# Optimization experiments

Hardware: AMD Instinct MI355X
Metric: run time of the kernel (lower is better)

The kernel has to match this reference:

```python
import jax, jax.numpy as jnp
import numpy as np

D_MODEL = 1024

def setup_inputs() -> dict:
    key = jax.random.key(0)
    ks = jax.random.split(key, 7)
    B, S, D = 4, 2048, D_MODEL
    scale = 1.0 / np.sqrt(D)
    x = jax.random.normal(ks[0], (B, S, D), dtype=jnp.float32)
    Wq = jax.random.normal(ks[1], (D, D), dtype=jnp.float32) * scale
    bq = jnp.zeros((D,), dtype=jnp.float32)
    Wk = jax.random.normal(ks[2], (D, D), dtype=jnp.float32) * scale
    bk = jnp.zeros((D,), dtype=jnp.float32)
    Wv = jax.random.normal(ks[3], (D, D), dtype=jnp.float32) * scale
    bv = jnp.zeros((D,), dtype=jnp.float32)
    return {"x": x, "Wq": Wq, "bq": bq, "Wk": Wk, "bk": bk, "Wv": Wv, "bv": bv}

def reference(x, Wq, bq, Wk, bk, Wv, bv):
    # Single-head attention; scale = 1/sqrt(d_model) as in the torch module (self.d_k = d_model).
    d_k = x.shape[-1]
    q = jnp.einsum('bsd,de->bse', x, Wq) + bq
    k = jnp.einsum('bsd,de->bse', x, Wk) + bk
    v = jnp.einsum('bsd,de->bse', x, Wv) + bv
    scores = jnp.einsum('bqd,bkd->bqk', q, k) / jnp.sqrt(jnp.asarray(d_k, x.dtype))
    attn = jax.nn.softmax(scores, axis=-1)
    return jnp.einsum('bqk,bkd->bqd', attn, v)
```

## Files before the change

kernel.cpp:

```cpp
#include <hip/hip_runtime.h>
#include <hip/hip_bf16.h>

#define DM 1024
#define SEQ 2048
#define NBATCH 4

using f32x4 = __attribute__((ext_vector_type(4))) float;
using s16x8 = __attribute__((ext_vector_type(8))) short;
using u16x4 = __attribute__((ext_vector_type(4))) unsigned short;
using u16x8 = __attribute__((ext_vector_type(8))) unsigned short;

__device__ __forceinline__ unsigned short f2bf(float f) {
  union { float f; unsigned u; } v; v.f = f;
  return (unsigned short)((v.u + 0x7fffu + ((v.u >> 16) & 1u)) >> 16);
}

__device__ __forceinline__ void gll16(const unsigned short* g, unsigned short* l) {
  __builtin_amdgcn_global_load_lds((const __attribute__((address_space(1))) void*)g,
                                   (__attribute__((address_space(3))) void*)l,
                                   16, 0, 0);
}

__global__ void prep_k(const float* __restrict__ X,
                       const float* __restrict__ Wq, const float* __restrict__ Wk,
                       const float* __restrict__ Wv,
                       unsigned short* __restrict__ XB, unsigned short* __restrict__ WT) {
  __shared__ float t[32][33];
  const int b = blockIdx.x;
  if (b < 4096) {
    const int i = b * 256 + threadIdx.x;
    const f32x4* p = (const f32x4*)X;
    f32x4 a = p[2 * i], c = p[2 * i + 1];
    u16x8 o;
#pragma unroll
    for (int q = 0; q < 4; q++) { o[q] = f2bf(a[q]); o[4 + q] = f2bf(c[q]); }
    *(u16x8*)(XB + (size_t)i * 8) = o;
  } else {
    const int r2 = b - 4096;
    const int seg = r2 >> 10;
    const int rem = r2 & 1023;
    const int k0 = (rem >> 5) * 32, n0 = (rem & 31) * 32;
    const float* W = (seg == 0) ? Wq : (seg == 1) ? Wk : Wv;
    unsigned short* out = WT + (size_t)seg * DM * DM;
    const int tr = threadIdx.x >> 5, tc = threadIdx.x & 31;
#pragma unroll
    for (int p = 0; p < 4; p++) {
      int r = tr + p * 8;
      t[r][tc] = W[(size_t)(k0 + r) * DM + n0 + tc];
    }
    __syncthreads();
#pragma unroll
    for (int p = 0; p < 4; p++) {
      int r = tr + p * 8;
      out[(size_t)(n0 + r) * DM + k0 + tc] = f2bf(t[tc][r]);
    }
  }
}

__global__ void combine_k(const float* __restrict__ ms, const float* __restrict__ ss,
                          float* __restrict__ T) {
  const int idx = blockIdx.x * 256 + threadIdx.x;
  const float* m = ms + (size_t)idx * 16;
  const float* s = ss + (size_t)idx * 32;
  float mv[16];
#pragma unroll
  for (int t = 0; t < 16; t++) mv[t] = m[t];
  float M = mv[0];
#pragma unroll
  for (int t = 1; t < 16; t++) M = fmaxf(M, mv[t]);
  float L = 0.f;
#pragma unroll
  for (int t = 0; t < 16; t++) L += (s[2 * t] + s[2 * t + 1]) * __expf(mv[t] - M);
  T[idx] = 1.0f;
#pragma unroll
  for (int t = 1; t < 16; t++) T[t * 8192 + idx] = __expf(mv[t - 1] - mv[t]);
  T[16 * 8192 + idx] = __expf(mv[15] - M) / L;
}

__global__ __launch_bounds__(512, 2) void qkv8_k(
    const unsigned short* __restrict__ A,
    const unsigned short* __restrict__ B,
    unsigned short* __restrict__ Qo, unsigned short* __restrict__ Ko,
    unsigned short* __restrict__ Vt,
    const float* __restrict__ bq, const float* __restrict__ bk,
    const float* __restrict__ bv) {
  constexpr int NKS = 32;
  __shared__ unsigned short lds8[65536];
  unsigned short* lA = lds8;
  unsigned short* lB = lds8 + 32768;

  const int tid = threadIdx.x;
  const int w = tid >> 6, l = tid & 63;
  const int ll = l & 15, qd = l >> 4;
  const int wm = w & 1, wn = w >> 1;

  const int bid = blockIdx.x;
  const int xcd = bid & 7, slot = bid >> 3;
  const int mt = xcd * 4 + slot / 12;
  const int nt = slot % 12;
  const int tileM = mt * 256, tileN = nt * 256;

  const int seg = l >> 3, ch = l & 7;
  const int rowo = seg * 2 + (ch >> 2);
  const int kc = (ch & 3) ^ (seg & 3);
  const unsigned short* gA0 = A + (size_t)(tileM + w * 16 + rowo) * DM + kc * 8;
  const unsigned short* gA1 = gA0 + (size_t)128 * DM;
  const unsigned short* gB0 = B + (size_t)(tileN + w * 16 + rowo) * DM + kc * 8;
  const unsigned short* gB1 = gB0 + (size_t)128 * DM;
  const int dA0 = w * 512, dA1 = (w + 8) * 512;

#define STAGE_A(n_) do { unsigned short* d_ = lA + ((n_) & 3) * 8192;          \
    gll16(gA0 + (size_t)(n_) * 32, d_ + dA0);                                  \
    gll16(gA1 + (size_t)(n_) * 32, d_ + dA1); } while (0)
#define STAGE_B(n_) do { unsigned short* d_ = lB + ((n_) & 3) * 8192;          \
    gll16(gB0 + (size_t)(n_) * 32, d_ + dA0);                                  \
    gll16(gB1 + (size_t)(n_) * 32, d_ + dA1); } while (0)

  const int Ra = wm * 128 + ll;
  const int aoff = (Ra >> 1) * 64 + ((Ra & 1) * 4 + (qd ^ ((Ra >> 1) & 3))) * 8;
  const int Rb = wn * 64 + ll;
  const int boff = (Rb >> 1) * 64 + ((Rb & 1) * 4 + (qd ^ ((Rb >> 1) & 3))) * 8;

  f32x4 acc[8][4];
#pragma unroll
  for (int i = 0; i < 8; i++)
#pragma unroll
    for (int j = 0; j < 4; j++) acc[i][j] = (f32x4){0.f, 0.f, 0.f, 0.f};

  STAGE_A(0); STAGE_B(0); STAGE_A(1); STAGE_B(1); STAGE_A(2); STAGE_B(2); STAGE_B(3);
  __builtin_amdgcn_sched_barrier(0);
  __builtin_amdgcn_s_waitcnt(0x0F7A);
  __builtin_amdgcn_sched_barrier(0);
  __builtin_amdgcn_s_barrier();
  __builtin_amdgcn_sched_barrier(0);

  for (int n = 0; n < NKS; ++n) {
    const unsigned short* sA = lA + (n & 3) * 8192;
    const unsigned short* sB = lB + (n & 3) * 8192;
    s16x8 af[4], bf[4];

#pragma unroll
    for (int i = 0; i < 4; i++) af[i] = *(const s16x8*)&sA[aoff + i * 512];
#pragma unroll
    for (int j = 0; j < 4; j++) bf[j] = *(const s16x8*)&sB[boff + j * 512];
    if (n + 3 < NKS) STAGE_A(n + 3);
    __builtin_amdgcn_sched_barrier(0);
    __builtin_amdgcn_s_barrier();
    __builtin_amdgcn_s_waitcnt(0xC07F);
    __builtin_amdgcn_sched_barrier(0);
    __builtin_amdgcn_s_setprio(1);
#pragma unroll
    for (int i = 0; i < 4; i++)
#pragma unroll
      for (int j = 0; j < 4; j++)
        acc[i][j] = __builtin_amdgcn_mfma_f32_16x16x32_bf16(af[i], bf[j], acc[i][j], 0, 0, 0);
    __builtin_amdgcn_s_setprio(0);
    __builtin_amdgcn_sched_barrier(0);
    __builtin_amdgcn_s_barrier();
    __builtin_amdgcn_sched_barrier(0);

#pragma unroll
    for (int i = 0; i < 4; i++) af[i] = *(const s16x8*)&sA[aoff + (i + 4) * 512];
    if (n + 4 < NKS) STAGE_B(n + 4);
    __builtin_amdgcn_sched_barrier(0);
    __builtin_amdgcn_s_barrier();
    __builtin_amdgcn_s_waitcnt(0xC07F);
    __builtin_amdgcn_sched_barrier(0);
    __builtin_amdgcn_s_setprio(1);
#pragma unroll
    for (int i = 0; i < 4; i++)
#pragma unroll
      for (int j = 0; j < 4; j++)
        acc[i + 4][j] = __builtin_amdgcn_mfma_f32_16x16x32_bf16(af[i], bf[j], acc[i + 4][j], 0, 0, 0);
    __builtin_amdgcn_s_setprio(0);
    if (n < NKS - 4)       __builtin_amdgcn_s_waitcnt(0x0F7A);
    else if (n == NKS - 4) __builtin_amdgcn_s_waitcnt(0x0F78);
    else if (n == NKS - 3) __builtin_amdgcn_s_waitcnt(0x0F74);
    else if (n == NKS - 2) __builtin_amdgcn_s_waitcnt(0x0F70);
    __builtin_amdgcn_sched_barrier(0);
    __builtin_amdgcn_s_barrier();
    __builtin_amdgcn_sched_barrier(0);
  }
#undef STAGE_A
#undef STAGE_B

#pragma unroll
  for (int i = 0; i < 8; i++) {
    const int gm0 = tileM + wm * 128 + i * 16 + qd * 4;
#pragma unroll
    for (int j = 0; j < 4; j++) {
      const int gn = tileN + wn * 64 + j * 16 + ll;
      const int seg2 = gn >> 10;
      const int colin = gn & 1023;
      if (seg2 == 0) {
        const float bias = bq[colin];
#pragma unroll
        for (int r = 0; r < 4; r++) Qo[(size_t)(gm0 + r) * DM + colin] = f2bf(acc[i][j][r] + bias);
      } else if (seg2 == 1) {
        const float bias = bk[colin];
#pragma unroll
        for (int r = 0; r < 4; r++) Ko[(size_t)(gm0 + r) * DM + colin] = f2bf(acc[i][j][r] + bias);
      } else {
        const float bias = bv[colin];
        u16x4 pk;
#pragma unroll
        for (int r = 0; r < 4; r++) pk[r] = f2bf(acc[i][j][r] + bias);
        const int b = gm0 >> 11, s0 = gm0 & 2047;
        *(u16x4*)(Vt + ((size_t)((b << 10) + colin)) * SEQ + s0) = pk;
      }
    }
  }
}

template <int MODE, int BM, int LDA, int LDB, int KDIM>
__global__ void gemm_nt(const unsigned short* __restrict__ A,
                        const unsigned short* __restrict__ B,
                        void* __restrict__ C0,
                        unsigned short* __restrict__ C1,
                        unsigned short* __restrict__ C2,
                        const float* __restrict__ bq,
                        const float* __restrict__ bk,
                        const float* __restrict__ bv,
                        float* __restrict__ sm,
                        float* __restrict__ sv,
                        const float* __restrict__ Tt) {
  constexpr int ASTEPS = BM / 32;
  constexpr int NJ = (BM == 128) ? 4 : 2;
  constexpr int WNOFF = 16 * NJ;
  __shared__ unsigned short lbuf[(BM + 128) * 64];
  __shared__ float fred[256];

  const int tid = threadIdx.x;
  const int w = tid >> 6;
  const int L = tid & 63;
  const int wm = (BM == 128) ? (w & 1) : 0;
  const int wn = (BM == 128) ? (w >> 1) : w;
  const int qd = L >> 4, ll = L & 15;

  const int bid = blockIdx.x;
  const int xcd = bid & 7, slot = bid >> 3;
  int bz, tileM, tileN, nT;
  if (MODE == 1) {
    bz = xcd >> 1;
    const int mh = xcd & 1;
    const int nloc = slot & 15, mloc = slot >> 4;
    tileM = (mh * 8 + mloc) * 128; tileN = nloc * 128; nT = nloc;
  } else {
    bz = xcd >> 1;
    const int mh = xcd & 1;
    const int nloc = slot & 7, mloc = slot >> 3;
    tileM = (mh * 16 + mloc) * 64; tileN = nloc * 128; nT = nloc;
  }
  (void)nT;

  const unsigned short* Ab = A;
  const unsigned short* Bb = B;
  if (MODE == 1) { Ab += (size_t)bz * SEQ * DM; Bb += (size_t)bz * SEQ * DM; }
  if (MODE == 2) { Ab += (size_t)bz * SEQ * SEQ; Bb += (size_t)bz * DM * SEQ; }

  const int srow = tid >> 3;
  const int pch = tid & 7;
  const int gch = pch ^ (srow & 7);
  const unsigned short* gA = Ab + (size_t)(tileM + srow) * LDA + gch * 8;
  const unsigned short* gB = Bb + (size_t)(tileN + srow) * LDB + gch * 8;
  unsigned short* lA = lbuf;
  unsigned short* lB = lbuf + BM * 64;
  unsigned short* wAp = &lA[srow * 64 + pch * 8];
  unsigned short* wBp = &lB[srow * 64 + pch * 8];

  u16x8 rA[ASTEPS], rB[4];
#define LOADT(kt) do {                                                         \
    const size_t kk_ = (size_t)(kt) * 64;                                      \
    _Pragma("unroll")                                                          \
    for (int i_ = 0; i_ < ASTEPS; i_++)                                        \
      rA[i_] = *(const u16x8*)(gA + (size_t)i_ * 32 * LDA + kk_);              \
    _Pragma("unroll")                                                          \
    for (int i_ = 0; i_ < 4; i_++)                                             \
      rB[i_] = *(const u16x8*)(gB + (size_t)i_ * 32 * LDB + kk_);              \
  } while (0)
#define WRITET() do {                                                          \
    _Pragma("unroll")                                                          \
    for (int i_ = 0; i_ < ASTEPS; i_++) *(u16x8*)(wAp + i_ * 32 * 64) = rA[i_];\
    _Pragma("unroll")                                                          \
    for (int i_ = 0; i_ < 4; i_++)      *(u16x8*)(wBp + i_ * 32 * 64) = rB[i_];\
  } while (0)

  f32x4 acc[4][NJ];
#pragma unroll
  for (int i = 0; i < 4; i++)
#pragma unroll
    for (int j = 0; j < NJ; j++) acc[i][j] = (f32x4){0.f, 0.f, 0.f, 0.f};

  const int sw = L & 7;

  float tTn[4][4];
  const float* Tb = nullptr;
  if (MODE == 2) {
    Tb = Tt + (size_t)bz * SEQ + tileM;
#pragma unroll
    for (int i = 0; i < 4; i++)
#pragma unroll
      for (int r = 0; r < 4; r++) tTn[i][r] = Tb[1 * 8192 + i * 16 + qd * 4 + r];
  }

  constexpr int NK = KDIM / 64;
  LOADT(0);
  WRITET();
  __syncthreads();

  for (int k = 0; k < NK; ++k) {
    if (MODE == 2 && k >= 2 && (k & 1) == 0) {
#pragma unroll
      for (int i = 0; i < 4; i++)
#pragma unroll
        for (int j = 0; j < NJ; j++)
#pragma unroll
          for (int r = 0; r < 4; r++) acc[i][j][r] *= tTn[i][r];
      const int tn = (k >> 1) + 1;
#pragma unroll
      for (int i = 0; i < 4; i++)
#pragma unroll
        for (int r = 0; r < 4; r++) tTn[i][r] = Tb[(size_t)tn * 8192 + i * 16 + qd * 4 + r];
    }

    if (k + 1 < NK) LOADT(k + 1);

#pragma unroll
    for (int s = 0; s < 2; s++) {
      const int pc = ((s * 4 + qd) ^ sw) * 8;
      s16x8 av[4], bv4[NJ];
#pragma unroll
      for (int i = 0; i < 4; i++)
        av[i] = *(const s16x8*)&lA[(wm * 64 + i * 16 + ll) * 64 + pc];
#pragma unroll
      for (int j = 0; j < NJ; j++)
        bv4[j] = *(const s16x8*)&lB[(wn * WNOFF + j * 16 + ll) * 64 + pc];
#pragma unroll
      for (int i = 0; i < 4; i++)
#pragma unroll
        for (int j = 0; j < NJ; j++)
          acc[i][j] = __builtin_amdgcn_mfma_f32_16x16x32_bf16(av[i], bv4[j], acc[i][j], 0, 0, 0);
    }

    if (k + 1 < NK) {
      __builtin_amdgcn_s_waitcnt(0xC07F);
      __builtin_amdgcn_sched_barrier(0);
      __builtin_amdgcn_s_barrier();
      __builtin_amdgcn_sched_barrier(0);
      WRITET();
      __syncthreads();
    }
  }
#undef LOADT
#undef WRITET

  if (MODE == 1) {
    __syncthreads();
    float mt[4][4];
#pragma unroll
    for (int i = 0; i < 4; i++)
#pragma unroll
      for (int r = 0; r < 4; r++) {
#pragma unroll
        for (int j = 0; j < NJ; j++) acc[i][j][r] *= 0.03125f;
        float v = fmaxf(fmaxf(acc[i][0][r], acc[i][1][r]), fmaxf(acc[i][2][r], acc[i][3][r]));
#pragma unroll
        for (int m = 1; m < 16; m <<= 1) v = fmaxf(v, __shfl_xor(v, m, 16));
        mt[i][r] = v;
      }
    if (ll == 0) {
#pragma unroll
      for (int i = 0; i < 4; i++)
#pragma unroll
        for (int r = 0; r < 4; r++)
          fred[wn * 128 + wm * 64 + i * 16 + qd * 4 + r] = mt[i][r];
    }
    __syncthreads();
#pragma unroll
    for (int i = 0; i < 4; i++)
#pragma unroll
      for (int r = 0; r < 4; r++) {
        const int row = wm * 64 + i * 16 + qd * 4 + r;
        mt[i][r] = fmaxf(fred[row], fred[128 + row]);
      }
#pragma unroll
    for (int i = 0; i < 4; i++)
#pragma unroll
      for (int r = 0; r < 4; r++) {
        const int row = wm * 64 + i * 16 + qd * 4 + r;
        float s = 0.f;
#pragma unroll
        for (int j = 0; j < NJ; j++) {
          float e = __expf(acc[i][j][r] - mt[i][r]);
          s += e;
          const int col = wn * WNOFF + j * 16 + ll;
          lbuf[row * 128 + ((((col >> 4) ^ (row & 7)) << 4) | (col & 15))] = f2bf(e);
        }
#pragma unroll
        for (int m = 1; m < 16; m <<= 1) s += __shfl_xor(s, m, 16);
        if (ll == 0) {
          const size_t base = (size_t)bz * SEQ + tileM + row;
          sv[base * 32 + nT * 2 + wn] = s;
          if (wn == 0) sm[base * 16 + nT] = mt[i][r];
        }
      }
    __syncthreads();
    unsigned short* P = (unsigned short*)C0 + (size_t)bz * SEQ * SEQ;
#pragma unroll
    for (int p = 0; p < 8; p++) {
      const int c = p * 256 + tid;
      const int row = c >> 4, cg = c & 15;
      const int phys = ((((cg >> 1) ^ (row & 7)) << 4) | ((cg & 1) << 3));
      u16x8 val = *(const u16x8*)&lbuf[row * 128 + phys];
      *(u16x8*)(P + (size_t)(tileM + row) * SEQ + tileN + cg * 8) = val;
    }
  } else if (MODE == 2) {
    float* O = (float*)C0 + (size_t)bz * SEQ * DM;
#pragma unroll
    for (int i = 0; i < 4; i++) {
      const int gm0 = tileM + i * 16 + qd * 4;
#pragma unroll
      for (int j = 0; j < NJ; j++) {
        const int gn = tileN + wn * WNOFF + j * 16 + ll;
#pragma unroll
        for (int r = 0; r < 4; r++)
          O[(size_t)(gm0 + r) * DM + gn] = acc[i][j][r] * tTn[i][r];
      }
    }
  }
  (void)bq; (void)bk; (void)bv; (void)C1; (void)C2;
}

extern "C" void kernel_launch(void* const* d_in, const int* in_sizes, int n_in,
                              void* d_out, int out_size, void* d_ws, size_t ws_size,
                              hipStream_t stream) {
  (void)in_sizes; (void)n_in; (void)out_size; (void)ws_size;
  const float* x  = (const float*)d_in[0];
  const float* Wq = (const float*)d_in[1];
  const float* bq = (const float*)d_in[2];
  const float* Wk = (const float*)d_in[3];
  const float* bk = (const float*)d_in[4];
  const float* Wv = (const float*)d_in[5];
  const float* bv = (const float*)d_in[6];
  float* out = (float*)d_out;
  char* ws = (char*)d_ws;
  unsigned short* xb = (unsigned short*)(ws + 0);
  unsigned short* wt = (unsigned short*)(ws + 16777216);
  unsigned short* qb = (unsigned short*)(ws + 23068672);
  unsigned short* kb = (unsigned short*)(ws + 39845888);
  unsigned short* vt = (unsigned short*)(ws + 56623104);
  unsigned short* P  = (unsigned short*)(ws + 73400320);
  float*          ms = (float*)(ws + 106954752);
  float*          ss = (float*)(ws + 107479040);
  float*          Tt = (float*)(ws + 108527616);

  prep_k<<<7168, 256, 0, stream>>>(x, Wq, Wk, Wv, xb, wt);
  qkv8_k<<<384, 512, 0, stream>>>(xb, wt, qb, kb, vt, bq, bk, bv);
  gemm_nt<1, 128, 1024, 1024, 1024><<<1024, 256, 0, stream>>>(
      qb, kb, (void*)P, nullptr, nullptr, nullptr, nullptr, nullptr, ms, ss, nullptr);
  combine_k<<<32, 256, 0, stream>>>(ms, ss, Tt);
  gemm_nt<2, 64, 2048, 2048, 2048><<<1024, 256, 0, stream>>>(
      P, vt, (void*)out, nullptr, nullptr, nullptr, nullptr, nullptr, nullptr, nullptr, Tt);
}
```

Baseline: 271.4 us.

## Shrink QKV GEMM tile to 256x128 and double-buffer register fragments

The fused QKV projection GEMM now uses 256x128 output tiles instead of 256x256, doubling the grid to 768 blocks and halving the per-thread accumulators. The main loop is restructured so that the LDS fragment reads for the next k-step go into a second register set while the current MFMAs run, with a single merged stage per step. The intent is better wave occupancy and load balance across the 256 CUs and less exposed LDS latency. The cost is lower data reuse per tile, meaning more global and LDS traffic per FLOP.

```diff
diff --git a/kernel.cpp b/kernel.cpp
--- a/kernel.cpp
+++ b/kernel.cpp
@@ -85,108 +85,107 @@
     const float* __restrict__ bq, const float* __restrict__ bk,
     const float* __restrict__ bv) {
   constexpr int NKS = 32;
-  __shared__ unsigned short lds8[65536];
+  __shared__ unsigned short lds8[49152];
   unsigned short* lA = lds8;
   unsigned short* lB = lds8 + 32768;
 
   const int tid = threadIdx.x;
   const int w = tid >> 6, l = tid & 63;
   const int ll = l & 15, qd = l >> 4;
-  const int wm = w & 1, wn = w >> 1;
+  const int wm = w >> 1, wn = w & 1;
 
   const int bid = blockIdx.x;
   const int xcd = bid & 7, slot = bid >> 3;
-  const int mt = xcd * 4 + slot / 12;
-  const int nt = slot % 12;
-  const int tileM = mt * 256, tileN = nt * 256;
+  const int mt = xcd * 4 + slot / 24;
+  const int nt = slot % 24;
+  const int tileM = mt * 256, tileN = nt * 128;
 
   const int seg = l >> 3, ch = l & 7;
   const int rowo = seg * 2 + (ch >> 2);
   const int kc = (ch & 3) ^ (seg & 3);
-  const unsigned short* gA0 = A + (size_t)(tileM + w * 16 + rowo) * DM + kc * 8;
-  const unsigned short* gA1 = gA0 + (size_t)128 * DM;
+  const unsigned short* gA0 = A + (size_t)(tileM + w * 32 + rowo) * DM + kc * 8;
   const unsigned short* gB0 = B + (size_t)(tileN + w * 16 + rowo) * DM + kc * 8;
-  const unsigned short* gB1 = gB0 + (size_t)128 * DM;
-  const int dA0 = w * 512, dA1 = (w + 8) * 512;
-
-#define STAGE_A(n_) do { unsigned short* d_ = lA + ((n_) & 3) * 8192;          \
-    gll16(gA0 + (size_t)(n_) * 32, d_ + dA0);                                  \
-    gll16(gA1 + (size_t)(n_) * 32, d_ + dA1); } while (0)
-#define STAGE_B(n_) do { unsigned short* d_ = lB + ((n_) & 3) * 8192;          \
-    gll16(gB0 + (size_t)(n_) * 32, d_ + dA0);                                  \
-    gll16(gB1 + (size_t)(n_) * 32, d_ + dA1); } while (0)
-
-  const int Ra = wm * 128 + ll;
+  const int dA0 = w * 1024, dB0 = w * 512;
+
+#define STAGE(np) do {                                                         \
+    unsigned short* dA_ = lA + ((np) & 3) * 8192 + dA0;                        \
+    unsigned short* dB_ = lB + ((np) & 3) * 4096 + dB0;                        \
+    const size_t ko_ = (size_t)(np) * 32;                                      \
+    gll16(gA0 + ko_, dA_);                                                     \
+    gll16(gA0 + (size_t)16 * DM + ko_, dA_ + 512);                             \
+    gll16(gB0 + ko_, dB_);                                                     \
+  } while (0)
+
+  const int Ra = wm * 64 + ll;
   const int aoff = (Ra >> 1) * 64 + ((Ra & 1) * 4 + (qd ^ ((Ra >> 1) & 3))) * 8;
   const int Rb = wn * 64 + ll;
   const int boff = (Rb >> 1) * 64 + ((Rb & 1) * 4 + (qd ^ ((Rb >> 1) & 3))) * 8;
 
-  f32x4 acc[8][4];
-#pragma unroll
-  for (int i = 0; i < 8; i++)
+#define RDSET(AF, BF, np) do {                                                 \
+    const unsigned short* sA_ = lA + ((np) & 3) * 8192;                        \
+    const unsigned short* sB_ = lB + ((np) & 3) * 4096;                        \
+    _Pragma("unroll")                                                          \
+    for (int i_ = 0; i_ < 4; i_++) AF[i_] = *(const s16x8*)&sA_[aoff + i_ * 512]; \
+    _Pragma("unroll")                                                          \
+    for (int j_ = 0; j_ < 4; j_++) BF[j_] = *(const s16x8*)&sB_[boff + j_ * 512]; \
+  } while (0)
+
+  f32x4 acc[4][4];
+#pragma unroll
+  for (int i = 0; i < 4; i++)
 #pragma unroll
     for (int j = 0; j < 4; j++) acc[i][j] = (f32x4){0.f, 0.f, 0.f, 0.f};
 
-  STAGE_A(0); STAGE_B(0); STAGE_A(1); STAGE_B(1); STAGE_A(2); STAGE_B(2); STAGE_B(3);
+  s16x8 af0[4], bf0[4], af1[4], bf1[4];
+
+  STAGE(0); STAGE(1); STAGE(2);
   __builtin_amdgcn_sched_barrier(0);
-  __builtin_amdgcn_s_waitcnt(0x0F7A);
+  __builtin_amdgcn_s_waitcnt(0x0F76);
   __builtin_amdgcn_sched_barrier(0);
   __builtin_amdgcn_s_barrier();
   __builtin_amdgcn_sched_barrier(0);
-
-  for (int n = 0; n < NKS; ++n) {
-    const unsigned short* sA = lA + (n & 3) * 8192;
-    const unsigned short* sB = lB + (n & 3) * 8192;
-    s16x8 af[4], bf[4];
-
-#pragma unroll
-    for (int i = 0; i < 4; i++) af[i] = *(const s16x8*)&sA[aoff + i * 512];
-#pragma unroll
-    for (int j = 0; j < 4; j++) bf[j] = *(const s16x8*)&sB[boff + j * 512];
-    if (n + 3 < NKS) STAGE_A(n + 3);
-    __builtin_amdgcn_sched_barrier(0);
-    __builtin_amdgcn_s_barrier();
-    __builtin_amdgcn_s_waitcnt(0xC07F);
-    __builtin_amdgcn_sched_barrier(0);
-    __builtin_amdgcn_s_setprio(1);
-#pragma unroll
-    for (int i = 0; i < 4; i++)
-#pragma unroll
-      for (int j = 0; j < 4; j++)
-        acc[i][j] = __builtin_amdgcn_mfma_f32_16x16x32_bf16(af[i], bf[j], acc[i][j], 0, 0, 0);
-    __builtin_amdgcn_s_setprio(0);
-    __builtin_amdgcn_sched_barrier(0);
-    __builtin_amdgcn_s_barrier();
-    __builtin_amdgcn_sched_barrier(0);
-
-#pragma unroll
-    for (int i = 0; i < 4; i++) af[i] = *(const s16x8*)&sA[aoff + (i + 4) * 512];
-    if (n + 4 < NKS) STAGE_B(n + 4);
-    __builtin_amdgcn_sched_barrier(0);
-    __builtin_amdgcn_s_barrier();
-    __builtin_amdgcn_s_waitcnt(0xC07F);
-    __builtin_amdgcn_sched_barrier(0);
-    __builtin_amdgcn_s_setprio(1);
-#pragma unroll
-    for (int i = 0; i < 4; i++)
-#pragma unroll
-      for (int j = 0; j < 4; j++)
-        acc[i + 4][j] = __builtin_amdgcn_mfma_f32_16x16x32_bf16(af[i], bf[j], acc[i + 4][j], 0, 0, 0);
-    __builtin_amdgcn_s_setprio(0);
-    if (n < NKS - 4)       __builtin_amdgcn_s_waitcnt(0x0F7A);
-    else if (n == NKS - 4) __builtin_amdgcn_s_waitcnt(0x0F78);
-    else if (n == NKS - 3) __builtin_amdgcn_s_waitcnt(0x0F74);
-    else if (n == NKS - 2) __builtin_amdgcn_s_waitcnt(0x0F70);
-    __builtin_amdgcn_sched_barrier(0);
-    __builtin_amdgcn_s_barrier();
-    __builtin_amdgcn_sched_barrier(0);
-  }
-#undef STAGE_A
-#undef STAGE_B
-
-#pragma unroll
-  for (int i = 0; i < 8; i++) {
-    const int gm0 = tileM + wm * 128 + i * 16 + qd * 4;
+  RDSET(af0, bf0, 0);
+
+#define PIPE_STEP(n_, CA, CB, NA, NB) do {                                     \
+    if ((n_) <= NKS - 3) {                                                     \
+      __builtin_amdgcn_s_waitcnt(0x0F73);                        \
+    } else if ((n_) == NKS - 2) {                                              \
+      __builtin_amdgcn_s_waitcnt(0x0F70);                        \
+    }                                                                          \
+    if ((n_) <= NKS - 2) {                                                     \
+      __builtin_amdgcn_sched_barrier(0);                                       \
+      __builtin_amdgcn_s_barrier();                                            \
+      __builtin_amdgcn_sched_barrier(0);                                       \
+    }                                                                          \
+    if ((n_) + 1 < NKS) RDSET(NA, NB, (n_) + 1);                               \
+    if ((n_) + 3 < NKS) STAGE((n_) + 3);                                       \
+    __builtin_amdgcn_sched_barrier(0);                                         \
+    if ((n_) + 1 < NKS) __builtin_amdgcn_s_waitcnt(0xC87F);    \
+    else                __builtin_amdgcn_s_waitcnt(0xC07F);    \
+    __builtin_amdgcn_sched_barrier(0);                                         \
+    __builtin_amdgcn_s_setprio(1);                                             \
+    _Pragma("unroll")                                                          \
+    for (int i_ = 0; i_ < 4; i_++)                                             \
+      _Pragma("unroll")                                                        \
+      for (int j_ = 0; j_ < 4; j_++)                                           \
+        acc[i_][j_] = __builtin_amdgcn_mfma_f32_16x16x32_bf16(                 \
+            CA[i_], CB[j_], acc[i_][j_], 0, 0, 0);                             \
+    __builtin_amdgcn_s_setprio(0);                                             \
+    __builtin_amdgcn_sched_barrier(0);                                         \
+  } while (0)
+
+#pragma unroll
+  for (int n = 0; n < NKS; n += 2) {
+    PIPE_STEP(n, af0, bf0, af1, bf1);
+    PIPE_STEP(n + 1, af1, bf1, af0, bf0);
+  }
+#undef PIPE_STEP
+#undef RDSET
+#undef STAGE
+
+#pragma unroll
+  for (int i = 0; i < 4; i++) {
+    const int gm0 = tileM + wm * 64 + i * 16 + qd * 4;
 #pragma unroll
     for (int j = 0; j < 4; j++) {
       const int gn = tileN + wn * 64 + j * 16 + ll;
@@ -455,7 +454,7 @@
   float*          Tt = (float*)(ws + 108527616);
 
   prep_k<<<7168, 256, 0, stream>>>(x, Wq, Wk, Wv, xb, wt);
-  qkv8_k<<<384, 512, 0, stream>>>(xb, wt, qb, kb, vt, bq, bk, bv);
+  qkv8_k<<<768, 512, 0, stream>>>(xb, wt, qb, kb, vt, bq, bk, bv);
   gemm_nt<1, 128, 1024, 1024, 1024><<<1024, 256, 0, stream>>>(
       qb, kb, (void*)P, nullptr, nullptr, nullptr, nullptr, nullptr, ms, ss, nullptr);
   combine_k<<<32, 256, 0, stream>>>(ms, ss, Tt);
```

Measured after the change: 249.1 us. 1.09x faster.
